# Performance work log

Measured on AMD Instinct MI355X. Metric: run time of the kernel, lower is better.

Reference implementation:

```python
import jax, jax.numpy as jnp
import numpy as np

VOCAB = 28996
EMBED = 512
N = 8192


def setup_inputs() -> dict:
    key = jax.random.key(0)
    k1, k2, k3, k4 = jax.random.split(key, 4)
    x = jax.random.normal(k1, (N, EMBED), dtype=jnp.float32)
    y = jax.random.randint(k2, (N,), 0, VOCAB, dtype=jnp.int64 if jax.config.jax_enable_x64 else jnp.int32)
    # nn.Linear params: weight (vocab, embed), bias (vocab,)
    W = jax.random.normal(k3, (VOCAB, EMBED), dtype=jnp.float32) * 0.02
    b = jax.random.normal(k4, (VOCAB,), dtype=jnp.float32) * 0.02
    return {"x": x, "y": y, "W": W, "b": b}


def reference(x, y, W, b):
    # Decoder: linear -> softmax over vocab (dim=1)
    logits = jnp.einsum("ne,ve->nv", x, W) + b          # (N, VOCAB)
    probs = jax.nn.softmax(logits, axis=1)              # first softmax (faithful to original)
    # nn.CrossEntropyLoss applied to probs: mean over nodes of
    #   logsumexp(probs) - probs[y]   (i.e., -log_softmax(probs)[y])
    logp = jax.nn.log_softmax(probs, axis=1)            # second (redundant) softmax pass
    nll = -jnp.take_along_axis(logp, y[:, None].astype(jnp.int32), axis=1)[:, 0]
    return jnp.mean(nll)
```

## Files before the change

kernel.cpp:

```cpp
#include <hip/hip_runtime.h>
#include <stdint.h>

#define VOCAB 28996
#define EMBED 512
#define NROWS 8192
#define VPAD  29056
#define LOG2E 1.4426950408889634f
#define WSCALE 16.0f
#define INV_WSCALE_L2E (LOG2E / 16.0f)

typedef __attribute__((ext_vector_type(4)))  int   i32x4;
typedef __attribute__((ext_vector_type(8)))  int   i32x8;
typedef __attribute__((ext_vector_type(16))) float f32x16;

__device__ __forceinline__ int pk_fp8x4(float a, float b, float c, float d) {
  int r = __builtin_amdgcn_cvt_pk_fp8_f32(a, b, 0, false);
  r = __builtin_amdgcn_cvt_pk_fp8_f32(c, d, r, true);
  return r;
}

__device__ __forceinline__ size_t tile_dst(int r, int o) {
  return (size_t)((r >> 5) * 8 + (o >> 6)) * 2048 +
         (((o >> 5) & 1) * 32 + (r & 31)) * 32 + (o & 31);
}

__global__ void __launch_bounds__(256)
prep_kernel(const float* __restrict__ x, const float* __restrict__ W,
            const float* __restrict__ b, const int* __restrict__ y,
            uint8_t* __restrict__ xT, uint8_t* __restrict__ wT,
            float* __restrict__ py, float* __restrict__ sg) {
  const int bid = blockIdx.x;
  if (bid < 7264) {
    int i = (bid * 256 + threadIdx.x) * 8;
    const int VK = VOCAB * EMBED;
    int2 o;
    if (i < VK) {
      float4 v0 = *(const float4*)(W + i);
      float4 v1 = *(const float4*)(W + i + 4);
      o.x = pk_fp8x4(v0.x * WSCALE, v0.y * WSCALE, v0.z * WSCALE, v0.w * WSCALE);
      o.y = pk_fp8x4(v1.x * WSCALE, v1.y * WSCALE, v1.z * WSCALE, v1.w * WSCALE);
    } else { o.x = 0; o.y = 0; }
    *(int2*)(wT + tile_dst(i >> 9, i & 511)) = o;
  } else if (bid < 9312) {
    int i = ((bid - 7264) * 256 + threadIdx.x) * 8;
    float4 v0 = *(const float4*)(x + i);
    float4 v1 = *(const float4*)(x + i + 4);
    int2 o;
    o.x = pk_fp8x4(v0.x, v0.y, v0.z, v0.w);
    o.y = pk_fp8x4(v1.x, v1.y, v1.z, v1.w);
    *(int2*)(xT + tile_dst(i >> 9, i & 511)) = o;
  } else if (bid < 11360) {
    const int row  = ((bid - 9312) * 256 + threadIdx.x) >> 6;
    const int lane = threadIdx.x & 63;
    const int yr = y[row];
    const float4* xr = (const float4*)(x + (size_t)row * EMBED);
    const float4* wr = (const float4*)(W + (size_t)yr * EMBED);
    float d = 0.f;
#pragma unroll
    for (int t = 0; t < 2; ++t) {
      float4 a = xr[lane * 2 + t], c = wr[lane * 2 + t];
      d += a.x * c.x + a.y * c.y + a.z * c.z + a.w * c.w;
    }
#pragma unroll
    for (int m = 1; m < 64; m <<= 1) d += __shfl_xor(d, m);
    if (lane == 0) py[row] = __expf(d + b[yr]);
  } else {
    int i = (bid - 11360) * 256 + threadIdx.x;
    sg[i] = 0.f;
  }
}

__global__ void __launch_bounds__(256, 3)
gemm_stats_kernel(const uint8_t* __restrict__ xT, const uint8_t* __restrict__ wT,
                  const float* __restrict__ bias, float* __restrict__ sg) {
  const int tid  = threadIdx.x;
  const int lane = tid & 63;
  const int w    = tid >> 6;
  const int l31  = lane & 31;
  const int h    = lane >> 5;
  const int wr   = (w >> 1) * 64;
  const int wc   = (w & 1) * 64;
  const int rowBase = blockIdx.x * 128;
  const int colBase = blockIdx.y * 128;

  const uint8_t* aT = xT + ((size_t)(((rowBase + wr) >> 5) * 8)) * 2048 + lane * 32;
  const uint8_t* bT = wT + ((size_t)(((colBase + wc) >> 5) * 8)) * 2048 + lane * 32;

  f32x16 acc[2][2];
#pragma unroll
  for (int i = 0; i < 2; ++i)
#pragma unroll
    for (int j = 0; j < 2; ++j)
#pragma unroll
      for (int r = 0; r < 16; ++r) acc[i][j][r] = 0.f;

#pragma unroll
  for (int s = 0; s < 8; ++s) {
    const int offs = s * 2048;
    i32x8 af[2], bq[2];
#pragma unroll
    for (int ii = 0; ii < 2; ++ii) {
      i32x4 lo = *(const i32x4*)(aT + ii * 16384 + offs);
      i32x4 hi = *(const i32x4*)(aT + ii * 16384 + offs + 16);
      af[ii] = __builtin_shufflevector(lo, hi, 0, 1, 2, 3, 4, 5, 6, 7);
    }
#pragma unroll
    for (int jj = 0; jj < 2; ++jj) {
      i32x4 lo = *(const i32x4*)(bT + jj * 16384 + offs);
      i32x4 hi = *(const i32x4*)(bT + jj * 16384 + offs + 16);
      bq[jj] = __builtin_shufflevector(lo, hi, 0, 1, 2, 3, 4, 5, 6, 7);
    }
#pragma unroll
    for (int ii = 0; ii < 2; ++ii)
#pragma unroll
      for (int jj = 0; jj < 2; ++jj)
        acc[ii][jj] = __builtin_amdgcn_mfma_scale_f32_32x32x64_f8f6f4(
            af[ii], bq[jj], acc[ii][jj], 0, 0, 0, 0x7F7F7F7F, 0, 0x7F7F7F7F);
  }

  float bvl[2];
#pragma unroll
  for (int jj = 0; jj < 2; ++jj) {
    const int col = colBase + wc + jj * 32 + l31;
    bvl[jj] = (col < VOCAB) ? bias[col] * LOG2E : -1e30f;
  }

  float sp[32];
#pragma unroll
  for (int ii = 0; ii < 2; ++ii)
#pragma unroll
    for (int r = 0; r < 16; ++r)
      sp[ii * 16 + r] = exp2f(fmaf(acc[ii][0][r], INV_WSCALE_L2E, bvl[0])) +
                        exp2f(fmaf(acc[ii][1][r], INV_WSCALE_L2E, bvl[1]));

  float t1[16];
#pragma unroll
  for (int u = 0; u < 16; ++u) {
    float a = sp[2 * u]     + __shfl_xor(sp[2 * u],     1);
    float b = sp[2 * u + 1] + __shfl_xor(sp[2 * u + 1], 1);
    t1[u] = (l31 & 1) ? b : a;
  }
  float t2[8];
#pragma unroll
  for (int u = 0; u < 8; ++u) {
    float a = t1[2 * u]     + __shfl_xor(t1[2 * u],     2);
    float b = t1[2 * u + 1] + __shfl_xor(t1[2 * u + 1], 2);
    t2[u] = (l31 & 2) ? b : a;
  }
  float t3[4];
#pragma unroll
  for (int u = 0; u < 4; ++u) {
    float a = t2[2 * u]     + __shfl_xor(t2[2 * u],     4);
    float b = t2[2 * u + 1] + __shfl_xor(t2[2 * u + 1], 4);
    t3[u] = (l31 & 4) ? b : a;
  }
  float t4[2];
#pragma unroll
  for (int u = 0; u < 2; ++u) {
    float a = t3[2 * u]     + __shfl_xor(t3[2 * u],     8);
    float b = t3[2 * u + 1] + __shfl_xor(t3[2 * u + 1], 8);
    t4[u] = (l31 & 8) ? b : a;
  }
  {
    float a = t4[0] + __shfl_xor(t4[0], 16);
    float b = t4[1] + __shfl_xor(t4[1], 16);
    float ssum = (l31 & 16) ? b : a;
    const int v = l31;
    const int row = rowBase + wr + (v >> 4) * 32 + (v & 3) + 8 * ((v & 15) >> 2) + 4 * h;
    atomicAdd(&sg[row], ssum);
  }
}

__global__ void finalize_kernel(const float* __restrict__ sg, const float* __restrict__ py,
                                float* __restrict__ out) {
  __shared__ float red[256];
  float a = 0.f;
  for (int i = threadIdx.x; i < NROWS; i += 256)
    a += py[i] / sg[i];
  red[threadIdx.x] = a;
  __syncthreads();
  for (int st = 128; st > 0; st >>= 1) {
    if (threadIdx.x < st) red[threadIdx.x] += red[threadIdx.x + st];
    __syncthreads();
  }
  if (threadIdx.x == 0)
    out[0] = logf((float)(VOCAB + 1)) - red[0] * (1.f / (float)NROWS);
}

extern "C" void kernel_launch(void* const* d_in, const int* in_sizes, int n_in,
                              void* d_out, int out_size, void* d_ws, size_t ws_size,
                              hipStream_t stream) {
  const float* x = (const float*)d_in[0];
  const int*   y = (const int*)d_in[1];
  const float* W = (const float*)d_in[2];
  const float* b = (const float*)d_in[3];

  char* ws = (char*)d_ws;
  uint8_t* xT = (uint8_t*)ws;
  uint8_t* wT = (uint8_t*)(ws + 4194304);
  float*   sg = (float*)(ws + 4194304 + 14876672);
  float*   py = sg + NROWS;

  prep_kernel<<<11392, 256, 0, stream>>>(x, W, b, y, xT, wT, py, sg);
  gemm_stats_kernel<<<dim3(64, 227), 256, 0, stream>>>(xT, wT, b, sg);
  finalize_kernel<<<1, 256, 0, stream>>>(sg, py, (float*)d_out);
}
```

Before: 281.7 us.

## Widen GEMM column tile to 256 and rewrite fp8 prep as tiled-output writes

The GEMM block tile grows from 128x128 to 128x256, so each wave now computes a 64x128 sub-tile with eight accumulators. This reuses each A fragment across four B fragments and halves the number of column blocks and the atomic adds into the row sums. The prep kernel is reorganised so each thread writes 16 contiguous fp8 bytes of the tiled layout and reads 16 floats from the source row, which changes the scatter write pattern into contiguous stores. The larger accumulator set raises register pressure, so launch bounds drop to 2 blocks per SM, and the vocab padding and workspace offsets grow to match.

```diff
diff --git a/kernel.cpp b/kernel.cpp
--- a/kernel.cpp
+++ b/kernel.cpp
@@ -4,7 +4,7 @@
 #define VOCAB 28996
 #define EMBED 512
 #define NROWS 8192
-#define VPAD  29056
+#define VPAD2 29184
 #define LOG2E 1.4426950408889634f
 #define WSCALE 16.0f
 #define INV_WSCALE_L2E (LOG2E / 16.0f)
@@ -19,10 +19,6 @@
   return r;
 }
 
-__device__ __forceinline__ size_t tile_dst(int r, int o) {
-  return (size_t)((r >> 5) * 8 + (o >> 6)) * 2048 +
-         (((o >> 5) & 1) * 32 + (r & 31)) * 32 + (o & 31);
-}
 
 __global__ void __launch_bounds__(256)
 prep_kernel(const float* __restrict__ x, const float* __restrict__ W,
@@ -30,27 +26,37 @@
             uint8_t* __restrict__ xT, uint8_t* __restrict__ wT,
             float* __restrict__ py, float* __restrict__ sg) {
   const int bid = blockIdx.x;
-  if (bid < 7264) {
-    int i = (bid * 256 + threadIdx.x) * 8;
-    const int VK = VOCAB * EMBED;
-    int2 o;
-    if (i < VK) {
-      float4 v0 = *(const float4*)(W + i);
-      float4 v1 = *(const float4*)(W + i + 4);
-      o.x = pk_fp8x4(v0.x * WSCALE, v0.y * WSCALE, v0.z * WSCALE, v0.w * WSCALE);
-      o.y = pk_fp8x4(v1.x * WSCALE, v1.y * WSCALE, v1.z * WSCALE, v1.w * WSCALE);
-    } else { o.x = 0; o.y = 0; }
-    *(int2*)(wT + tile_dst(i >> 9, i & 511)) = o;
-  } else if (bid < 9312) {
-    int i = ((bid - 7264) * 256 + threadIdx.x) * 8;
-    float4 v0 = *(const float4*)(x + i);
-    float4 v1 = *(const float4*)(x + i + 4);
-    int2 o;
-    o.x = pk_fp8x4(v0.x, v0.y, v0.z, v0.w);
-    o.y = pk_fp8x4(v1.x, v1.y, v1.z, v1.w);
-    *(int2*)(xT + tile_dst(i >> 9, i & 511)) = o;
-  } else if (bid < 11360) {
-    const int row  = ((bid - 9312) * 256 + threadIdx.x) >> 6;
+  if (bid < 4672) {
+    const bool isW = bid < 3648;
+    const size_t beta = ((size_t)(isW ? bid : bid - 3648) * 256 + threadIdx.x) * 16;
+    const int tileIdx = (int)(beta >> 11);
+    const int om  = (int)(beta & 2047);
+    const int g = tileIdx >> 3, s = tileIdx & 7;
+    const int lam = om >> 5, c0 = om & 31;
+    const int row = g * 32 + (lam & 31);
+    const int k0  = s * 64 + (lam >> 5) * 32 + c0;
+    int4 o;
+    if (isW) {
+      if (row < VOCAB) {
+        const float4* src = (const float4*)(W + (size_t)row * EMBED + k0);
+        float4 v0 = src[0], v1 = src[1], v2 = src[2], v3 = src[3];
+        o.x = pk_fp8x4(v0.x * WSCALE, v0.y * WSCALE, v0.z * WSCALE, v0.w * WSCALE);
+        o.y = pk_fp8x4(v1.x * WSCALE, v1.y * WSCALE, v1.z * WSCALE, v1.w * WSCALE);
+        o.z = pk_fp8x4(v2.x * WSCALE, v2.y * WSCALE, v2.z * WSCALE, v2.w * WSCALE);
+        o.w = pk_fp8x4(v3.x * WSCALE, v3.y * WSCALE, v3.z * WSCALE, v3.w * WSCALE);
+      } else { o.x = 0; o.y = 0; o.z = 0; o.w = 0; }
+      *(int4*)(wT + beta) = o;
+    } else {
+      const float4* src = (const float4*)(x + (size_t)row * EMBED + k0);
+      float4 v0 = src[0], v1 = src[1], v2 = src[2], v3 = src[3];
+      o.x = pk_fp8x4(v0.x, v0.y, v0.z, v0.w);
+      o.y = pk_fp8x4(v1.x, v1.y, v1.z, v1.w);
+      o.z = pk_fp8x4(v2.x, v2.y, v2.z, v2.w);
+      o.w = pk_fp8x4(v3.x, v3.y, v3.z, v3.w);
+      *(int4*)(xT + beta) = o;
+    }
+  } else if (bid < 6720) {
+    const int row  = ((bid - 4672) * 256 + threadIdx.x) >> 6;
     const int lane = threadIdx.x & 63;
     const int yr = y[row];
     const float4* xr = (const float4*)(x + (size_t)row * EMBED);
@@ -65,12 +71,12 @@
     for (int m = 1; m < 64; m <<= 1) d += __shfl_xor(d, m);
     if (lane == 0) py[row] = __expf(d + b[yr]);
   } else {
-    int i = (bid - 11360) * 256 + threadIdx.x;
+    int i = (bid - 6720) * 256 + threadIdx.x;
     sg[i] = 0.f;
   }
 }
 
-__global__ void __launch_bounds__(256, 3)
+__global__ void __launch_bounds__(256, 2)
 gemm_stats_kernel(const uint8_t* __restrict__ xT, const uint8_t* __restrict__ wT,
                   const float* __restrict__ bias, float* __restrict__ sg) {
   const int tid  = threadIdx.x;
@@ -79,25 +85,25 @@
   const int l31  = lane & 31;
   const int h    = lane >> 5;
   const int wr   = (w >> 1) * 64;
-  const int wc   = (w & 1) * 64;
+  const int wc   = (w & 1) * 128;
   const int rowBase = blockIdx.x * 128;
-  const int colBase = blockIdx.y * 128;
+  const int colBase = blockIdx.y * 256;
 
   const uint8_t* aT = xT + ((size_t)(((rowBase + wr) >> 5) * 8)) * 2048 + lane * 32;
   const uint8_t* bT = wT + ((size_t)(((colBase + wc) >> 5) * 8)) * 2048 + lane * 32;
 
-  f32x16 acc[2][2];
+  f32x16 acc[2][4];
 #pragma unroll
   for (int i = 0; i < 2; ++i)
 #pragma unroll
-    for (int j = 0; j < 2; ++j)
+    for (int j = 0; j < 4; ++j)
 #pragma unroll
       for (int r = 0; r < 16; ++r) acc[i][j][r] = 0.f;
 
 #pragma unroll
   for (int s = 0; s < 8; ++s) {
     const int offs = s * 2048;
-    i32x8 af[2], bq[2];
+    i32x8 af[2], bq[4];
 #pragma unroll
     for (int ii = 0; ii < 2; ++ii) {
       i32x4 lo = *(const i32x4*)(aT + ii * 16384 + offs);
@@ -105,7 +111,7 @@
       af[ii] = __builtin_shufflevector(lo, hi, 0, 1, 2, 3, 4, 5, 6, 7);
     }
 #pragma unroll
-    for (int jj = 0; jj < 2; ++jj) {
+    for (int jj = 0; jj < 4; ++jj) {
       i32x4 lo = *(const i32x4*)(bT + jj * 16384 + offs);
       i32x4 hi = *(const i32x4*)(bT + jj * 16384 + offs + 16);
       bq[jj] = __builtin_shufflevector(lo, hi, 0, 1, 2, 3, 4, 5, 6, 7);
@@ -113,14 +119,14 @@
 #pragma unroll
     for (int ii = 0; ii < 2; ++ii)
 #pragma unroll
-      for (int jj = 0; jj < 2; ++jj)
+      for (int jj = 0; jj < 4; ++jj)
         acc[ii][jj] = __builtin_amdgcn_mfma_scale_f32_32x32x64_f8f6f4(
             af[ii], bq[jj], acc[ii][jj], 0, 0, 0, 0x7F7F7F7F, 0, 0x7F7F7F7F);
   }
 
-  float bvl[2];
-#pragma unroll
-  for (int jj = 0; jj < 2; ++jj) {
+  float bvl[4];
+#pragma unroll
+  for (int jj = 0; jj < 4; ++jj) {
     const int col = colBase + wc + jj * 32 + l31;
     bvl[jj] = (col < VOCAB) ? bias[col] * LOG2E : -1e30f;
   }
@@ -129,9 +135,13 @@
 #pragma unroll
   for (int ii = 0; ii < 2; ++ii)
 #pragma unroll
-    for (int r = 0; r < 16; ++r)
-      sp[ii * 16 + r] = exp2f(fmaf(acc[ii][0][r], INV_WSCALE_L2E, bvl[0])) +
-                        exp2f(fmaf(acc[ii][1][r], INV_WSCALE_L2E, bvl[1]));
+    for (int r = 0; r < 16; ++r) {
+      float e = 0.f;
+#pragma unroll
+      for (int jj = 0; jj < 4; ++jj)
+        e += exp2f(fmaf(acc[ii][jj][r], INV_WSCALE_L2E, bvl[jj]));
+      sp[ii * 16 + r] = e;
+    }
 
   float t1[16];
 #pragma unroll
@@ -198,10 +208,10 @@
   char* ws = (char*)d_ws;
   uint8_t* xT = (uint8_t*)ws;
   uint8_t* wT = (uint8_t*)(ws + 4194304);
-  float*   sg = (float*)(ws + 4194304 + 14876672);
+  float*   sg = (float*)(ws + 4194304 + 14942208);
   float*   py = sg + NROWS;
 
-  prep_kernel<<<11392, 256, 0, stream>>>(x, W, b, y, xT, wT, py, sg);
-  gemm_stats_kernel<<<dim3(64, 227), 256, 0, stream>>>(xT, wT, b, sg);
+  prep_kernel<<<6752, 256, 0, stream>>>(x, W, b, y, xT, wT, py, sg);
+  gemm_stats_kernel<<<dim3(64, 114), 256, 0, stream>>>(xT, wT, b, sg);
   finalize_kernel<<<1, 256, 0, stream>>>(sg, py, (float*)d_out);
 }
```

Result: slower. 291.8 us (+3.6%).
